# Kernel tuning notes

Hardware: AMD Instinct MI355X
Metric: run time of the kernel (lower is better)

## Reference

```python
import jax, jax.numpy as jnp
import numpy as np

MAX_DISP = 48


def setup_inputs() -> dict:
    key = jax.random.key(0)
    k1, k2 = jax.random.split(key)
    b, c, h, w = 8, 128, 96, 320
    left_feature = jax.random.normal(k1, (b, c, h, w), dtype=jnp.float32)
    right_feature = jax.random.normal(k2, (b, c, h, w), dtype=jnp.float32)
    return {"left_feature": left_feature, "right_feature": right_feature}


def reference(left_feature, right_feature):
    # Correlation cost volume: cost[b, i, h, x] = mean_c left[b,c,h,x] * right[b,c,h,x-i]
    # for x >= i, zero elsewhere. Loop is over the fixed disparity count (48),
    # each iteration touching only the valid width slice (honors the sparsity
    # structure of the original; no [b,c,h,D,w] intermediate is materialized).
    b, c, h, w = left_feature.shape
    slices = []
    for i in range(MAX_DISP):
        if i > 0:
            corr = (left_feature[:, :, :, i:] * right_feature[:, :, :, : w - i]).mean(axis=1)
            corr = jnp.pad(corr, ((0, 0), (0, 0), (i, 0)))  # zeros for x < i
        else:
            corr = (left_feature * right_feature).mean(axis=1)
        slices.append(corr)
    return jnp.stack(slices, axis=1)  # (b, max_disp, h, w)
```

## Files before the change

### kernel.cpp

```cpp
#include <hip/hip_runtime.h>
#include <stdint.h>


typedef __bf16 bf16x8 __attribute__((ext_vector_type(8)));
typedef float floatx16 __attribute__((ext_vector_type(16)));

constexpr int W = 320, H = 96, C = 128, NB = 8, MAXD = 48;
constexpr int HW = H * W;
constexpr int SC = 16;
constexpr int MATD = 8 * W;
constexpr int BUFD = 2 * MATD;
constexpr int NST = C / SC;

__device__ __forceinline__ uint32_t pack_bf16x2(float a, float b) {
    uint32_t ua = __float_as_uint(a), ub = __float_as_uint(b);
    uint32_t lo = (ua + 0x7fffu + ((ua >> 16) & 1u)) >> 16;
    uint32_t hi = (ub + 0x7fffu + ((ub >> 16) & 1u)) & 0xffff0000u;
    return hi | lo;
}

__device__ __forceinline__ void soft_barrier() {
    asm volatile("s_waitcnt lgkmcnt(0)" ::: "memory");
    __builtin_amdgcn_s_barrier();
    asm volatile("" ::: "memory");
}

__global__ __launch_bounds__(640, 5) void cost_volume_kernel(
    const float* __restrict__ Lg, const float* __restrict__ Rg,
    float* __restrict__ out)
{
    __shared__ uint32_t lds[15840];

    const int t    = threadIdx.x;
    const int lane = t & 63;
    const int p    = t >> 6;
    const int n    = lane & 31;
    const int half = lane >> 5;

    const int b = blockIdx.x / H;
    const int h = blockIdx.x % H;
    const int baseLR = b * (C * HW) + h * W;

    const int rp = t / 80;
    const int c4 = t % 80;
    const float* Lt = Lg + baseLR + 2 * rp * HW + 4 * c4;
    const float* Rt = Rg + baseLR + 2 * rp * HW + 4 * c4;

    float4 l0, l1, r0, r1;

    auto loadStage = [&](int s) {
        const float* Lp = Lt + s * SC * HW;
        const float* Rp = Rt + s * SC * HW;
        l0 = *(const float4*)(Lp);
        l1 = *(const float4*)(Lp + HW);
        r0 = *(const float4*)(Rp);
        r1 = *(const float4*)(Rp + HW);
    };

    auto writeLDS = [&](uint32_t* buf) {
        uint32_t* d = buf + rp * W + 4 * c4;
        uint4 v;
        v.x = pack_bf16x2(l0.x, l1.x);
        v.y = pack_bf16x2(l0.y, l1.y);
        v.z = pack_bf16x2(l0.z, l1.z);
        v.w = pack_bf16x2(l0.w, l1.w);
        *reinterpret_cast<uint4*>(d) = v;
        v.x = pack_bf16x2(r0.x, r1.x);
        v.y = pack_bf16x2(r0.y, r1.y);
        v.z = pack_bf16x2(r0.z, r1.z);
        v.w = pack_bf16x2(r0.w, r1.w);
        *reinterpret_cast<uint4*>(d + MATD) = v;
    };

    floatx16 acc0 = 0.f, acc1 = 0.f, acc2 = 0.f;

    loadStage(0);
    writeLDS(lds);
    loadStage(1);
    soft_barrier();

#pragma unroll 1
    for (int s = 0; s < NST; ++s) {
        const uint32_t* sL = lds + (s & 1) * BUFD;
        const uint32_t* sR = sL + MATD;

        const uint32_t* pa = sL + half * 4 * W + p * 32 + n;
        uint4 a4;
        a4.x = pa[0 * W]; a4.y = pa[1 * W]; a4.z = pa[2 * W]; a4.w = pa[3 * W];
        bf16x8 af = __builtin_bit_cast(bf16x8, a4);

        {
            const uint32_t* pb = sR + half * 4 * W + p * 32 + n;
            uint4 b4;
            b4.x = pb[0 * W]; b4.y = pb[1 * W]; b4.z = pb[2 * W]; b4.w = pb[3 * W];
            acc0 = __builtin_amdgcn_mfma_f32_32x32x16_bf16(
                af, __builtin_bit_cast(bf16x8, b4), acc0, 0, 0, 0);
        }
        if (p >= 1) {
            const uint32_t* pb = sR + half * 4 * W + (p - 1) * 32 + n;
            uint4 b4;
            b4.x = pb[0 * W]; b4.y = pb[1 * W]; b4.z = pb[2 * W]; b4.w = pb[3 * W];
            acc1 = __builtin_amdgcn_mfma_f32_32x32x16_bf16(
                af, __builtin_bit_cast(bf16x8, b4), acc1, 0, 0, 0);
        }
        if (p >= 2) {
            const uint32_t* pb = sR + half * 4 * W + (p - 2) * 32 + n;
            uint4 b4;
            b4.x = pb[0 * W]; b4.y = pb[1 * W]; b4.z = pb[2 * W]; b4.w = pb[3 * W];
            acc2 = __builtin_amdgcn_mfma_f32_32x32x16_bf16(
                af, __builtin_bit_cast(bf16x8, b4), acc2, 0, 0, 0);
        }

        if (s < NST - 1) writeLDS(lds + ((s + 1) & 1) * BUFD);
        if (s < NST - 2) loadStage(s + 2);
        soft_barrier();
    }

    __syncthreads();

    float* sS = reinterpret_cast<float*>(lds) + p * (MAXD * 33);
    const int ob = b * (MAXD * HW) + h * W + p * 32;
    constexpr float scale = 1.f / 128.f;

    if (p < 2) {
        for (int e = lane; e < MAXD * 33; e += 64) sS[e] = 0.f;
    }

#define FILL_TILE(DP, ACC)                                                  \
    if (p >= (DP)) {                                                        \
        _Pragma("unroll")                                                   \
        for (int r = 0; r < 16; ++r) {                                      \
            int m = (r & 3) + 8 * (r >> 2) + 4 * half;                      \
            int i = 32 * (DP) + m - n;                                      \
            if (i >= 0 && i < MAXD)                                         \
                sS[i * 33 + m] = ACC[r] * scale;                            \
        }                                                                   \
    }
    FILL_TILE(0, acc0)
    FILL_TILE(1, acc1)
    FILL_TILE(2, acc2)
#undef FILL_TILE

#pragma unroll
    for (int e = 0; e < 24; ++e) {
        int idx = e * 64 + lane;
        int i = idx >> 5;
        int m = idx & 31;
        out[ob + i * HW + m] = sS[i * 33 + m];
    }
}

extern "C" void kernel_launch(void* const* d_in, const int* in_sizes, int n_in,
                              void* d_out, int out_size, void* d_ws, size_t ws_size,
                              hipStream_t stream) {
    const float* L = (const float*)d_in[0];
    const float* R = (const float*)d_in[1];
    float* out = (float*)d_out;
    cost_volume_kernel<<<dim3(NB * H), dim3(640), 0, stream>>>(L, R, out);
}
```

Baseline: 276.2 us.

## Stream right features via global_load_lds DMA and convert to bf16 at read

```diff
diff --git a/kernel.cpp b/kernel.cpp
--- a/kernel.cpp
+++ b/kernel.cpp
@@ -8,9 +8,10 @@
 constexpr int W = 320, H = 96, C = 128, NB = 8, MAXD = 48;
 constexpr int HW = H * W;
 constexpr int SC = 16;
-constexpr int MATD = 8 * W;
-constexpr int BUFD = 2 * MATD;
 constexpr int NST = C / SC;
+constexpr int LBD = (SC / 2) * W;
+constexpr int ROFF = 2 * LBD;
+constexpr int RBD = SC * W;
 
 __device__ __forceinline__ uint32_t pack_bf16x2(float a, float b) {
     uint32_t ua = __float_as_uint(a), ub = __float_as_uint(b);
@@ -19,11 +20,15 @@
     return hi | lo;
 }
 
-__device__ __forceinline__ void soft_barrier() {
-    asm volatile("s_waitcnt lgkmcnt(0)" ::: "memory");
-    __builtin_amdgcn_s_barrier();
-    asm volatile("" ::: "memory");
+__device__ __forceinline__ floatx16 mfma_bf16(bf16x8 a, uint4 b, floatx16 c) {
+    return __builtin_amdgcn_mfma_f32_32x32x16_bf16(
+        a, __builtin_bit_cast(bf16x8, b), c, 0, 0, 0);
 }
+
+#define GLDS(gp, lp, SZ)                                                   \
+    __builtin_amdgcn_global_load_lds(                                      \
+        (const __attribute__((address_space(1))) void*)(gp),               \
+        (__attribute__((address_space(3))) void*)(lp), SZ, 0, 0)
 
 __global__ __launch_bounds__(640, 5) void cost_volume_kernel(
     const float* __restrict__ Lg, const float* __restrict__ Rg,
@@ -44,76 +49,97 @@
     const int rp = t / 80;
     const int c4 = t % 80;
     const float* Lt = Lg + baseLR + 2 * rp * HW + 4 * c4;
-    const float* Rt = Rg + baseLR + 2 * rp * HW + 4 * c4;
 
-    float4 l0, l1, r0, r1;
-
-    auto loadStage = [&](int s) {
+    float4 l0, l1;
+    auto loadL = [&](int s) {
         const float* Lp = Lt + s * SC * HW;
-        const float* Rp = Rt + s * SC * HW;
         l0 = *(const float4*)(Lp);
         l1 = *(const float4*)(Lp + HW);
-        r0 = *(const float4*)(Rp);
-        r1 = *(const float4*)(Rp + HW);
     };
-
-    auto writeLDS = [&](uint32_t* buf) {
-        uint32_t* d = buf + rp * W + 4 * c4;
+    auto writeL = [&](int s) {
+        uint32_t* d = lds + (s & 1) * LBD + rp * W + 4 * c4;
         uint4 v;
         v.x = pack_bf16x2(l0.x, l1.x);
         v.y = pack_bf16x2(l0.y, l1.y);
         v.z = pack_bf16x2(l0.z, l1.z);
         v.w = pack_bf16x2(l0.w, l1.w);
         *reinterpret_cast<uint4*>(d) = v;
-        v.x = pack_bf16x2(r0.x, r1.x);
-        v.y = pack_bf16x2(r0.y, r1.y);
-        v.z = pack_bf16x2(r0.z, r1.z);
-        v.w = pack_bf16x2(r0.w, r1.w);
-        *reinterpret_cast<uint4*>(d + MATD) = v;
+    };
+
+    const int r0 = p & 7;
+    auto dmaR = [&](int s) {
+#pragma unroll
+        for (int rr = 0; rr < 2; ++rr) {
+            const int row = r0 + rr * 8;
+            const float* g = Rg + baseLR + (s * SC + row) * HW;
+            uint32_t* l = lds + ROFF + (s & 1) * RBD + row * W;
+            GLDS(g + lane * 4, l, 16);
+            GLDS(g + 256 + lane, l + 256, 4);
+        }
     };
 
     floatx16 acc0 = 0.f, acc1 = 0.f, acc2 = 0.f;
 
-    loadStage(0);
-    writeLDS(lds);
-    loadStage(1);
-    soft_barrier();
+    loadL(0);
+    dmaR(0);
+    asm volatile("s_waitcnt vmcnt(4)" ::: "memory");
+    writeL(0);
+    loadL(1);
 
-#pragma unroll 1
+#pragma unroll
     for (int s = 0; s < NST; ++s) {
-        const uint32_t* sL = lds + (s & 1) * BUFD;
-        const uint32_t* sR = sL + MATD;
+        if (s + 1 < NST) {
+            dmaR(s + 1);
+            asm volatile("s_waitcnt vmcnt(6) lgkmcnt(0)" ::: "memory");
+        } else {
+            asm volatile("s_waitcnt vmcnt(0) lgkmcnt(0)" ::: "memory");
+        }
+        __builtin_amdgcn_s_barrier();
+        asm volatile("" ::: "memory");
 
-        const uint32_t* pa = sL + half * 4 * W + p * 32 + n;
+        const uint32_t* La = lds + (s & 1) * LBD + half * (4 * W) + p * 32 + n;
         uint4 a4;
-        a4.x = pa[0 * W]; a4.y = pa[1 * W]; a4.z = pa[2 * W]; a4.w = pa[3 * W];
+        a4.x = La[0 * W]; a4.y = La[1 * W]; a4.z = La[2 * W]; a4.w = La[3 * W];
         bf16x8 af = __builtin_bit_cast(bf16x8, a4);
 
+        const float* Rf = reinterpret_cast<const float*>(lds + ROFF + (s & 1) * RBD)
+                        + half * (8 * W) + n;
         {
-            const uint32_t* pb = sR + half * 4 * W + p * 32 + n;
+            const float* pb = Rf + 32 * p;
             uint4 b4;
-            b4.x = pb[0 * W]; b4.y = pb[1 * W]; b4.z = pb[2 * W]; b4.w = pb[3 * W];
-            acc0 = __builtin_amdgcn_mfma_f32_32x32x16_bf16(
-                af, __builtin_bit_cast(bf16x8, b4), acc0, 0, 0, 0);
+            b4.x = pack_bf16x2(pb[0 * W], pb[1 * W]);
+            b4.y = pack_bf16x2(pb[2 * W], pb[3 * W]);
+            b4.z = pack_bf16x2(pb[4 * W], pb[5 * W]);
+            b4.w = pack_bf16x2(pb[6 * W], pb[7 * W]);
+            acc0 = mfma_bf16(af, b4, acc0);
         }
         if (p >= 1) {
-            const uint32_t* pb = sR + half * 4 * W + (p - 1) * 32 + n;
+            const float* pb = Rf + 32 * (p - 1);
             uint4 b4;
-            b4.x = pb[0 * W]; b4.y = pb[1 * W]; b4.z = pb[2 * W]; b4.w = pb[3 * W];
-            acc1 = __builtin_amdgcn_mfma_f32_32x32x16_bf16(
-                af, __builtin_bit_cast(bf16x8, b4), acc1, 0, 0, 0);
+            b4.x = pack_bf16x2(pb[0 * W], pb[1 * W]);
+            b4.y = pack_bf16x2(pb[2 * W], pb[3 * W]);
+            b4.z = pack_bf16x2(pb[4 * W], pb[5 * W]);
+            b4.w = pack_bf16x2(pb[6 * W], pb[7 * W]);
+            acc1 = mfma_bf16(af, b4, acc1);
         }
         if (p >= 2) {
-            const uint32_t* pb = sR + half * 4 * W + (p - 2) * 32 + n;
+            const float* pb = Rf + 32 * (p - 2);
             uint4 b4;
-            b4.x = pb[0 * W]; b4.y = pb[1 * W]; b4.z = pb[2 * W]; b4.w = pb[3 * W];
-            acc2 = __builtin_amdgcn_mfma_f32_32x32x16_bf16(
-                af, __builtin_bit_cast(bf16x8, b4), acc2, 0, 0, 0);
+            b4.x = pack_bf16x2(pb[0 * W], pb[1 * W]);
+            b4.y = pack_bf16x2(pb[2 * W], pb[3 * W]);
+            b4.z = pack_bf16x2(pb[4 * W], pb[5 * W]);
+            b4.w = pack_bf16x2(pb[6 * W], pb[7 * W]);
+            acc2 = mfma_bf16(af, b4, acc2);
         }
 
-        if (s < NST - 1) writeLDS(lds + ((s + 1) & 1) * BUFD);
-        if (s < NST - 2) loadStage(s + 2);
-        soft_barrier();
+        if (s + 1 < NST) {
+            asm volatile("s_waitcnt vmcnt(4)" ::: "memory");
+            writeL(s + 1);
+            if (s + 2 < NST) loadL(s + 2);
+        }
+        asm volatile("s_waitcnt lgkmcnt(0)" ::: "memory");
+        __builtin_amdgcn_s_barrier();
+        asm volatile("" ::: "memory");
     }
 
     __syncthreads();
```

Measured after the change: 275.7 us. Within noise of the previous version (-0.2%).

## Shrink LDS footprint via chunked epilogue, raise occupancy, and reorder MFMA after prefetch

Applied to the files above, without the earlier changes.

```diff
diff --git a/kernel.cpp b/kernel.cpp
--- a/kernel.cpp
+++ b/kernel.cpp
@@ -11,6 +11,8 @@
 constexpr int MATD = 8 * W;
 constexpr int BUFD = 2 * MATD;
 constexpr int NST = C / SC;
+constexpr int ECH = 24;
+constexpr int ESZ = ECH * 33;
 
 __device__ __forceinline__ uint32_t pack_bf16x2(float a, float b) {
     uint32_t ua = __float_as_uint(a), ub = __float_as_uint(b);
@@ -25,11 +27,11 @@
     asm volatile("" ::: "memory");
 }
 
-__global__ __launch_bounds__(640, 5) void cost_volume_kernel(
+__global__ __launch_bounds__(640, 8) void cost_volume_kernel(
     const float* __restrict__ Lg, const float* __restrict__ Rg,
     float* __restrict__ out)
 {
-    __shared__ uint32_t lds[15840];
+    __shared__ uint32_t lds[2 * BUFD];
 
     const int t    = threadIdx.x;
     const int lane = t & 63;
@@ -89,64 +91,71 @@
         a4.x = pa[0 * W]; a4.y = pa[1 * W]; a4.z = pa[2 * W]; a4.w = pa[3 * W];
         bf16x8 af = __builtin_bit_cast(bf16x8, a4);
 
+        uint4 b40, b41, b42;
         {
             const uint32_t* pb = sR + half * 4 * W + p * 32 + n;
-            uint4 b4;
-            b4.x = pb[0 * W]; b4.y = pb[1 * W]; b4.z = pb[2 * W]; b4.w = pb[3 * W];
-            acc0 = __builtin_amdgcn_mfma_f32_32x32x16_bf16(
-                af, __builtin_bit_cast(bf16x8, b4), acc0, 0, 0, 0);
+            b40.x = pb[0 * W]; b40.y = pb[1 * W]; b40.z = pb[2 * W]; b40.w = pb[3 * W];
         }
         if (p >= 1) {
             const uint32_t* pb = sR + half * 4 * W + (p - 1) * 32 + n;
-            uint4 b4;
-            b4.x = pb[0 * W]; b4.y = pb[1 * W]; b4.z = pb[2 * W]; b4.w = pb[3 * W];
-            acc1 = __builtin_amdgcn_mfma_f32_32x32x16_bf16(
-                af, __builtin_bit_cast(bf16x8, b4), acc1, 0, 0, 0);
+            b41.x = pb[0 * W]; b41.y = pb[1 * W]; b41.z = pb[2 * W]; b41.w = pb[3 * W];
         }
         if (p >= 2) {
             const uint32_t* pb = sR + half * 4 * W + (p - 2) * 32 + n;
-            uint4 b4;
-            b4.x = pb[0 * W]; b4.y = pb[1 * W]; b4.z = pb[2 * W]; b4.w = pb[3 * W];
-            acc2 = __builtin_amdgcn_mfma_f32_32x32x16_bf16(
-                af, __builtin_bit_cast(bf16x8, b4), acc2, 0, 0, 0);
+            b42.x = pb[0 * W]; b42.y = pb[1 * W]; b42.z = pb[2 * W]; b42.w = pb[3 * W];
         }
 
         if (s < NST - 1) writeLDS(lds + ((s + 1) & 1) * BUFD);
         if (s < NST - 2) loadStage(s + 2);
+
+        acc0 = __builtin_amdgcn_mfma_f32_32x32x16_bf16(
+            af, __builtin_bit_cast(bf16x8, b40), acc0, 0, 0, 0);
+        if (p >= 1)
+            acc1 = __builtin_amdgcn_mfma_f32_32x32x16_bf16(
+                af, __builtin_bit_cast(bf16x8, b41), acc1, 0, 0, 0);
+        if (p >= 2)
+            acc2 = __builtin_amdgcn_mfma_f32_32x32x16_bf16(
+                af, __builtin_bit_cast(bf16x8, b42), acc2, 0, 0, 0);
+
         soft_barrier();
     }
 
     __syncthreads();
 
-    float* sS = reinterpret_cast<float*>(lds) + p * (MAXD * 33);
+    float* sS = reinterpret_cast<float*>(lds) + p * ESZ;
     const int ob = b * (MAXD * HW) + h * W + p * 32;
     constexpr float scale = 1.f / 128.f;
 
-    if (p < 2) {
-        for (int e = lane; e < MAXD * 33; e += 64) sS[e] = 0.f;
-    }
+#pragma unroll 1
+    for (int k = 0; k < MAXD / ECH; ++k) {
+        if (k) asm volatile("s_waitcnt lgkmcnt(0)" ::: "memory");
+
+        if (p < 2) {
+            for (int e = lane; e < ESZ; e += 64) sS[e] = 0.f;
+        }
 
 #define FILL_TILE(DP, ACC)                                                  \
-    if (p >= (DP)) {                                                        \
-        _Pragma("unroll")                                                   \
-        for (int r = 0; r < 16; ++r) {                                      \
-            int m = (r & 3) + 8 * (r >> 2) + 4 * half;                      \
-            int i = 32 * (DP) + m - n;                                      \
-            if (i >= 0 && i < MAXD)                                         \
-                sS[i * 33 + m] = ACC[r] * scale;                            \
-        }                                                                   \
-    }
-    FILL_TILE(0, acc0)
-    FILL_TILE(1, acc1)
-    FILL_TILE(2, acc2)
+        if (p >= (DP)) {                                                    \
+            _Pragma("unroll")                                               \
+            for (int r = 0; r < 16; ++r) {                                  \
+                int m = (r & 3) + 8 * (r >> 2) + 4 * half;                  \
+                int il = 32 * (DP) + m - n - ECH * k;                       \
+                if (il >= 0 && il < ECH)                                    \
+                    sS[il * 33 + m] = ACC[r] * scale;                       \
+            }                                                               \
+        }
+        FILL_TILE(0, acc0)
+        FILL_TILE(1, acc1)
+        FILL_TILE(2, acc2)
 #undef FILL_TILE
 
 #pragma unroll
-    for (int e = 0; e < 24; ++e) {
-        int idx = e * 64 + lane;
-        int i = idx >> 5;
-        int m = idx & 31;
-        out[ob + i * HW + m] = sS[i * 33 + m];
+        for (int e = 0; e < ECH * 32 / 64; ++e) {
+            int idx = e * 64 + lane;
+            int il = idx >> 5;
+            int m  = idx & 31;
+            out[ob + (ECH * k + il) * HW + m] = sS[il * 33 + m];
+        }
     }
 }
 
```

Result: slower. 430.0 us (+55.7%).

## Load MFMA operands directly from global memory per wave, dropping LDS staging

Applied to the files above, without the earlier changes.

```diff
diff --git a/kernel.cpp b/kernel.cpp
--- a/kernel.cpp
+++ b/kernel.cpp
@@ -8,9 +8,11 @@
 constexpr int W = 320, H = 96, C = 128, NB = 8, MAXD = 48;
 constexpr int HW = H * W;
 constexpr int SC = 16;
-constexpr int MATD = 8 * W;
-constexpr int BUFD = 2 * MATD;
 constexpr int NST = C / SC;
+constexpr int TPP = W / 32;
+constexpr int NTASK = NB * H * TPP;
+constexpr int WPB = 4;
+constexpr int ESZ = MAXD * 33;
 
 __device__ __forceinline__ uint32_t pack_bf16x2(float a, float b) {
     uint32_t ua = __float_as_uint(a), ub = __float_as_uint(b);
@@ -19,111 +21,86 @@
     return hi | lo;
 }
 
-__device__ __forceinline__ void soft_barrier() {
-    asm volatile("s_waitcnt lgkmcnt(0)" ::: "memory");
-    __builtin_amdgcn_s_barrier();
-    asm volatile("" ::: "memory");
+__device__ __forceinline__ bf16x8 packf(const float* v) {
+    uint4 q;
+    q.x = pack_bf16x2(v[0], v[1]);
+    q.y = pack_bf16x2(v[2], v[3]);
+    q.z = pack_bf16x2(v[4], v[5]);
+    q.w = pack_bf16x2(v[6], v[7]);
+    return __builtin_bit_cast(bf16x8, q);
 }
 
-__global__ __launch_bounds__(640, 5) void cost_volume_kernel(
+__global__ __launch_bounds__(256, 3) void cost_volume_kernel(
     const float* __restrict__ Lg, const float* __restrict__ Rg,
     float* __restrict__ out)
 {
-    __shared__ uint32_t lds[15840];
+    __shared__ float scr[WPB * ESZ];
 
     const int t    = threadIdx.x;
     const int lane = t & 63;
-    const int p    = t >> 6;
+    const int w    = t >> 6;
     const int n    = lane & 31;
     const int half = lane >> 5;
 
-    const int b = blockIdx.x / H;
-    const int h = blockIdx.x % H;
+    const int wid   = blockIdx.x * WPB + w;
+    const int plane = wid / TPP;
+    const int p     = wid % TPP;
+    const int b     = plane / H;
+    const int h     = plane % H;
+
     const int baseLR = b * (C * HW) + h * W;
+    const int lofs = (8 * half) * HW + p * 32 + n;
+    const float* Ap  = Lg + baseLR + lofs;
+    const float* Bp0 = Rg + baseLR + lofs;
+    const float* Bp1 = Bp0 - 32;
+    const float* Bp2 = Bp0 - 64;
 
-    const int rp = t / 80;
-    const int c4 = t % 80;
-    const float* Lt = Lg + baseLR + 2 * rp * HW + 4 * c4;
-    const float* Rt = Rg + baseLR + 2 * rp * HW + 4 * c4;
+    float a_[2][8], b0_[2][8], b1_[2][8], b2_[2][8];
 
-    float4 l0, l1, r0, r1;
-
-    auto loadStage = [&](int s) {
-        const float* Lp = Lt + s * SC * HW;
-        const float* Rp = Rt + s * SC * HW;
-        l0 = *(const float4*)(Lp);
-        l1 = *(const float4*)(Lp + HW);
-        r0 = *(const float4*)(Rp);
-        r1 = *(const float4*)(Rp + HW);
-    };
-
-    auto writeLDS = [&](uint32_t* buf) {
-        uint32_t* d = buf + rp * W + 4 * c4;
-        uint4 v;
-        v.x = pack_bf16x2(l0.x, l1.x);
-        v.y = pack_bf16x2(l0.y, l1.y);
-        v.z = pack_bf16x2(l0.z, l1.z);
-        v.w = pack_bf16x2(l0.w, l1.w);
-        *reinterpret_cast<uint4*>(d) = v;
-        v.x = pack_bf16x2(r0.x, r1.x);
-        v.y = pack_bf16x2(r0.y, r1.y);
-        v.z = pack_bf16x2(r0.z, r1.z);
-        v.w = pack_bf16x2(r0.w, r1.w);
-        *reinterpret_cast<uint4*>(d + MATD) = v;
-    };
+#define LOAD_STAGE(BUF, S)                                                  \
+    {                                                                       \
+        const int o = (S) * SC * HW;                                        \
+        _Pragma("unroll")                                                   \
+        for (int j = 0; j < 8; ++j) a_[BUF][j] = Ap[o + j * HW];            \
+        _Pragma("unroll")                                                   \
+        for (int j = 0; j < 8; ++j) b0_[BUF][j] = Bp0[o + j * HW];          \
+        if (p >= 1) {                                                       \
+            _Pragma("unroll")                                               \
+            for (int j = 0; j < 8; ++j) b1_[BUF][j] = Bp1[o + j * HW];      \
+        }                                                                   \
+        if (p >= 2) {                                                       \
+            _Pragma("unroll")                                               \
+            for (int j = 0; j < 8; ++j) b2_[BUF][j] = Bp2[o + j * HW];      \
+        }                                                                   \
+    }
 
     floatx16 acc0 = 0.f, acc1 = 0.f, acc2 = 0.f;
 
-    loadStage(0);
-    writeLDS(lds);
-    loadStage(1);
-    soft_barrier();
+    LOAD_STAGE(0, 0)
 
-#pragma unroll 1
+#pragma unroll
     for (int s = 0; s < NST; ++s) {
-        const uint32_t* sL = lds + (s & 1) * BUFD;
-        const uint32_t* sR = sL + MATD;
+        const int cur = s & 1;
+        const int nxt = cur ^ 1;
+        if (s + 1 < NST) LOAD_STAGE(nxt, s + 1)
+        bf16x8 af = packf(a_[cur]);
+        acc0 = __builtin_amdgcn_mfma_f32_32x32x16_bf16(
+            af, packf(b0_[cur]), acc0, 0, 0, 0);
+        if (p >= 1)
+            acc1 = __builtin_amdgcn_mfma_f32_32x32x16_bf16(
+                af, packf(b1_[cur]), acc1, 0, 0, 0);
+        if (p >= 2)
+            acc2 = __builtin_amdgcn_mfma_f32_32x32x16_bf16(
+                af, packf(b2_[cur]), acc2, 0, 0, 0);
+    }
+#undef LOAD_STAGE
 
-        const uint32_t* pa = sL + half * 4 * W + p * 32 + n;
-        uint4 a4;
-        a4.x = pa[0 * W]; a4.y = pa[1 * W]; a4.z = pa[2 * W]; a4.w = pa[3 * W];
-        bf16x8 af = __builtin_bit_cast(bf16x8, a4);
-
-        {
-            const uint32_t* pb = sR + half * 4 * W + p * 32 + n;
-            uint4 b4;
-            b4.x = pb[0 * W]; b4.y = pb[1 * W]; b4.z = pb[2 * W]; b4.w = pb[3 * W];
-            acc0 = __builtin_amdgcn_mfma_f32_32x32x16_bf16(
-                af, __builtin_bit_cast(bf16x8, b4), acc0, 0, 0, 0);
-        }
-        if (p >= 1) {
-            const uint32_t* pb = sR + half * 4 * W + (p - 1) * 32 + n;
-            uint4 b4;
-            b4.x = pb[0 * W]; b4.y = pb[1 * W]; b4.z = pb[2 * W]; b4.w = pb[3 * W];
-            acc1 = __builtin_amdgcn_mfma_f32_32x32x16_bf16(
-                af, __builtin_bit_cast(bf16x8, b4), acc1, 0, 0, 0);
-        }
-        if (p >= 2) {
-            const uint32_t* pb = sR + half * 4 * W + (p - 2) * 32 + n;
-            uint4 b4;
-            b4.x = pb[0 * W]; b4.y = pb[1 * W]; b4.z = pb[2 * W]; b4.w = pb[3 * W];
-            acc2 = __builtin_amdgcn_mfma_f32_32x32x16_bf16(
-                af, __builtin_bit_cast(bf16x8, b4), acc2, 0, 0, 0);
-        }
-
-        if (s < NST - 1) writeLDS(lds + ((s + 1) & 1) * BUFD);
-        if (s < NST - 2) loadStage(s + 2);
-        soft_barrier();
-    }
-
-    __syncthreads();
-
-    float* sS = reinterpret_cast<float*>(lds) + p * (MAXD * 33);
+    float* sS = scr + w * ESZ;
     const int ob = b * (MAXD * HW) + h * W + p * 32;
     constexpr float scale = 1.f / 128.f;
 
     if (p < 2) {
-        for (int e = lane; e < MAXD * 33; e += 64) sS[e] = 0.f;
+        for (int e = lane; e < ESZ; e += 64) sS[e] = 0.f;
     }
 
 #define FILL_TILE(DP, ACC)                                                  \
@@ -156,5 +133,5 @@
     const float* L = (const float*)d_in[0];
     const float* R = (const float*)d_in[1];
     float* out = (float*)d_out;
-    cost_volume_kernel<<<dim3(NB * H), dim3(640), 0, stream>>>(L, R, out);
+    cost_volume_kernel<<<dim3(NTASK / WPB), dim3(64 * WPB), 0, stream>>>(L, R, out);
 }
```

New measurement: 275.9 us. Within noise of the previous version (-0.1%).
